# Performance work log

Measured on AMD Instinct MI355X. Metric: run time of the kernel, lower is better.

## Reference

```python
import jax, jax.numpy as jnp
import numpy as np


def setup_inputs() -> dict:
    key = jax.random.key(0)
    ks = jax.random.split(key, 5)
    b, l, ns, ni, d = 128, 64, 32, 16, 256
    scale = 1.0 / np.sqrt(d)
    return {
        "token_features": jax.random.normal(ks[0], (b, l, d), jnp.float32),
        "w_route_ws": jax.random.normal(ks[1], (l, ns, d), jnp.float32) * scale,
        "w_pose_ws": jax.random.normal(ks[2], (l, ns, d, d), jnp.float32) * scale,
        "w_route_si": jax.random.normal(ks[3], (ns, ni, d), jnp.float32) * scale,
        "w_pose_si": jax.random.normal(ks[4], (ns, ni, d, d), jnp.float32) * scale,
    }


def reference(token_features, w_route_ws, w_pose_ws, w_route_si, w_pose_si):
    d_model = token_features.shape[-1]

    # ---- route words -> slots ----
    # token activations ('norm' strategy): mean over d_model -> (b, l)
    a_words = jnp.sum(token_features, axis=-1) / d_model
    # routing logits (b, l, n_slot_caps), softmax over slot caps
    c_ws = jax.nn.softmax(jnp.einsum('lnj,blj->bln', w_route_ws, token_features), axis=-1)
    weighted_c = jnp.einsum('bls,bl->bs', c_ws, a_words)            # (b, ns)
    a_slots = weighted_c / jnp.sum(a_words, axis=-1, keepdims=True)  # (b, ns)
    # pose votes (b, l, ns, d) then weighted aggregation + divisive normalization
    u_hat_slots = jnp.einsum('lnij,blj->blni', w_pose_ws, token_features)
    u_slots = jnp.einsum('bls,bl,blsk->bsk', c_ws, a_words, u_hat_slots) / weighted_c[:, :, None]

    # ---- route slots -> intents ----
    c_si = jax.nn.softmax(jnp.einsum('sij,bsj->bsi', w_route_si, u_slots), axis=-1)
    weighted_c2 = jnp.einsum('bsi,bs->bi', c_si, a_slots)            # (b, ni)
    a_intents = weighted_c2 / jnp.sum(a_slots, axis=-1, keepdims=True)
    u_hat_intents = jnp.einsum('sijk,bsk->bsik', w_pose_si, u_slots)  # (b, ns, ni, d)
    u_intents = jnp.einsum('bsi,bs,bsik->bik', c_si, a_slots, u_hat_intents) / weighted_c2[:, :, None]

    return a_slots, u_slots, a_intents, u_intents
```

## Files before the change

kernel.cpp:

```cpp
#include <hip/hip_runtime.h>
#include <math.h>

#define B  128
#define L  64
#define NS 32
#define NI 16
#define D  256

typedef __attribute__((ext_vector_type(8))) short bf16x8;
typedef __attribute__((ext_vector_type(4))) float f32x4;

__device__ __forceinline__ float wave_reduce_sum(float v) {
#pragma unroll
  for (int off = 32; off; off >>= 1) v += __shfl_xor(v, off, 64);
  return v;
}
__device__ __forceinline__ float wave_reduce_max(float v) {
#pragma unroll
  for (int off = 32; off; off >>= 1) v = fmaxf(v, __shfl_xor(v, off, 64));
  return v;
}

__device__ __forceinline__ uint cvt_pk_bf16(float a, float b) {
  uint r;
  asm("v_cvt_pk_bf16_f32 %0, %1, %2" : "=v"(r) : "v"(a), "v"(b));
  return r;
}
__device__ __forceinline__ void split4(float4 v, uint2& h, uint2& lo) {
  h.x = cvt_pk_bf16(v.x, v.y);
  h.y = cvt_pk_bf16(v.z, v.w);
  float h0 = __uint_as_float(h.x << 16);
  float h1 = __uint_as_float(h.x & 0xFFFF0000u);
  float h2 = __uint_as_float(h.y << 16);
  float h3 = __uint_as_float(h.y & 0xFFFF0000u);
  lo.x = cvt_pk_bf16(v.x - h0, v.y - h1);
  lo.y = cvt_pk_bf16(v.z - h2, v.w - h3);
}

__device__ __forceinline__ void dma16(const void* g, void* l) {
  __builtin_amdgcn_global_load_lds(
      (const __attribute__((address_space(1))) void*)g,
      (__attribute__((address_space(3))) void*)l, 16, 0, 0);
}

__device__ __forceinline__ int swzA(int row, int kcol) {
  int byte = (row << 7) + (kcol << 1);
  byte ^= (row & 7) << 4;
  return byte >> 1;
}

__global__ __launch_bounds__(256) void kx_split(
    const float* __restrict__ tf, ushort* __restrict__ xh,
    ushort* __restrict__ xl) {
  int tile = blockIdx.x;
  int l  = tile >> 2;
  int jc = (tile & 3) * 64;
  int t  = threadIdx.x;
  int row = t >> 1;
  int k0  = (t & 1) * 32;
  const float* src = tf + ((size_t)row * L + l) * D + jc + k0;
  ushort* ht = xh + (size_t)tile * 8192;
  ushort* lt = xl + (size_t)tile * 8192;
#pragma unroll
  for (int c = 0; c < 8; ++c) {
    float4 v = *(const float4*)(src + c * 4);
    uint2 h, lo;
    split4(v, h, lo);
    int ix = swzA(row, k0 + c * 4);
    *(uint2*)&ht[ix] = h;
    *(uint2*)&lt[ix] = lo;
  }
}

__global__ __launch_bounds__(256) void k1_route_words(
    const float* __restrict__ tf, const float* __restrict__ wr,
    float* __restrict__ wlsT, float* __restrict__ a_words) {
  int bl = blockIdx.x;
  int b  = bl >> 6;
  int l  = bl & (L - 1);
  int t  = threadIdx.x;
  int wave = t >> 6, lane = t & 63;
  __shared__ float sx[D];
  __shared__ float slog[NS];
  __shared__ float s_aw;
  sx[t] = tf[bl * D + t];
  __syncthreads();
  const float* wbase = wr + l * NS * D;
#pragma unroll
  for (int r = 0; r < 8; ++r) {
    int n = wave * 8 + r;
    const float* w = wbase + n * D;
    float p = 0.f;
#pragma unroll
    for (int jj = 0; jj < 4; ++jj) {
      int j = lane + jj * 64;
      p = fmaf(w[j], sx[j], p);
    }
    p = wave_reduce_sum(p);
    if (lane == 0) slog[n] = p;
  }
  if (wave == 0) {
    float p = sx[lane] + sx[lane + 64] + sx[lane + 128] + sx[lane + 192];
    p = wave_reduce_sum(p);
    if (lane == 0) s_aw = p * (1.f / D);
  }
  __syncthreads();
  if (wave == 0) {
    float aw = s_aw;
    float v = (lane < NS) ? slog[lane] : -INFINITY;
    float m = wave_reduce_max(v);
    float e = (lane < NS) ? __expf(v - m) : 0.f;
    float s = wave_reduce_sum(e);
    if (lane < NS) wlsT[(l * NS + lane) * B + b] = (e / s) * aw;
    if (lane == 0) a_words[bl] = aw;
  }
}

__global__ __launch_bounds__(64) void k2_slots_agg(
    const float* __restrict__ wlsT, const float* __restrict__ a_words,
    float* __restrict__ weighted_c, float* __restrict__ a_slots) {
  int b = blockIdx.x;
  int lane = threadIdx.x;
  float aw = a_words[b * L + lane];
  float sa = wave_reduce_sum(aw);
  if (lane < NS) {
    float wc = 0.f;
    for (int l = 0; l < L; ++l) wc += wlsT[(l * NS + lane) * B + b];
    weighted_c[b * NS + lane] = wc;
    a_slots[b * NS + lane] = wc / sa;
  }
}

__global__ __launch_bounds__(256) void k3_mfma(
    const ushort* __restrict__ xh, const ushort* __restrict__ xl,
    const float* __restrict__ wp, const float* __restrict__ wlsT,
    float* __restrict__ part, int nsplit) {
  __shared__ ushort Ah[8192], Al[8192];
  __shared__ float sw[128];

  int bx  = blockIdx.x;
  int sp  = bx % nsplit;
  int rem = bx / nsplit;
  int it  = rem & 3;
  int s   = rem >> 2;
  int i0  = it * 64;
  int lchunk = L / nsplit;
  int l0     = sp * lchunk;
  int steps  = lchunk * 4;

  int t = threadIdx.x;
  int lane = t & 63, wv = t >> 6;
  int wm = wv >> 1, wn = wv & 1;
  int fr = lane & 15, q = lane >> 4;

  f32x4 P[4][2], R[4][2];
#pragma unroll
  for (int mi = 0; mi < 4; ++mi)
#pragma unroll
    for (int ni = 0; ni < 2; ++ni) { P[mi][ni] = (f32x4)0.f; R[mi][ni] = (f32x4)0.f; }

  for (int step = 0; step < steps; ++step) {
    int l   = l0 + (step >> 2);
    int jci = step & 3;
    size_t tile = ((size_t)l * 4 + jci) * 8192;
    const ushort* th = xh + tile;
    const ushort* tl = xl + tile;
#pragma unroll
    for (int ii = 0; ii < 4; ++ii) {
      int ofs = (wv * 4 + ii) * 512;
      dma16(th + ofs + lane * 8, &Ah[ofs]);
      dma16(tl + ofs + lane * 8, &Al[ofs]);
    }
    int jc = jci * 64;
    float4 rW[8];
    const float* wb = wp + ((size_t)l * NS + s) * (D * D) + jc + q * 8;
#pragma unroll
    for (int ni = 0; ni < 2; ++ni) {
      const float* wr_ = wb + (size_t)(i0 + wn * 32 + ni * 16 + fr) * D;
#pragma unroll
      for (int k2 = 0; k2 < 2; ++k2) {
        rW[(ni * 2 + k2) * 2 + 0] = *(const float4*)(wr_ + k2 * 32);
        rW[(ni * 2 + k2) * 2 + 1] = *(const float4*)(wr_ + k2 * 32 + 4);
      }
    }
    if (jci == 0 && t < 128) sw[t] = wlsT[((size_t)l * NS + s) * B + t];
    __syncthreads();

    bf16x8 bh[2][2], bl[2][2];
#pragma unroll
    for (int ni = 0; ni < 2; ++ni)
#pragma unroll
      for (int k2 = 0; k2 < 2; ++k2) {
        uint2 h0, e0, h1, e1;
        split4(rW[(ni * 2 + k2) * 2 + 0], h0, e0);
        split4(rW[(ni * 2 + k2) * 2 + 1], h1, e1);
        uint4 hu = {h0.x, h0.y, h1.x, h1.y};
        uint4 lu = {e0.x, e0.y, e1.x, e1.y};
        bh[ni][k2] = __builtin_bit_cast(bf16x8, hu);
        bl[ni][k2] = __builtin_bit_cast(bf16x8, lu);
      }
#pragma unroll
    for (int k2 = 0; k2 < 2; ++k2) {
      int kb = k2 * 32 + q * 8;
#pragma unroll
      for (int mi = 0; mi < 4; ++mi) {
        int ix = swzA(wm * 64 + mi * 16 + fr, kb);
        bf16x8 ah = *(const bf16x8*)&Ah[ix];
        bf16x8 al = *(const bf16x8*)&Al[ix];
#pragma unroll
        for (int ni = 0; ni < 2; ++ni) {
          P[mi][ni] = __builtin_amdgcn_mfma_f32_16x16x32_bf16(ah, bh[ni][k2], P[mi][ni], 0, 0, 0);
          P[mi][ni] = __builtin_amdgcn_mfma_f32_16x16x32_bf16(ah, bl[ni][k2], P[mi][ni], 0, 0, 0);
          P[mi][ni] = __builtin_amdgcn_mfma_f32_16x16x32_bf16(al, bh[ni][k2], P[mi][ni], 0, 0, 0);
        }
      }
    }
    if (jci == 3) {
#pragma unroll
      for (int mi = 0; mi < 4; ++mi) {
        f32x4 s4 = *(const f32x4*)&sw[wm * 64 + mi * 16 + q * 4];
#pragma unroll
        for (int ni = 0; ni < 2; ++ni) {
          R[mi][ni] += s4 * P[mi][ni];
          P[mi][ni] = (f32x4)0.f;
        }
      }
    }
    __syncthreads();
  }

  float* pout = part + ((size_t)sp * NS + s) * (B * D);
#pragma unroll
  for (int mi = 0; mi < 4; ++mi)
#pragma unroll
    for (int ni = 0; ni < 2; ++ni) {
      int col = i0 + wn * 32 + ni * 16 + fr;
#pragma unroll
      for (int r = 0; r < 4; ++r) {
        int bb = wm * 64 + mi * 16 + q * 4 + r;
        pout[(size_t)bb * D + col] = R[mi][ni][r];
      }
    }
}

__global__ __launch_bounds__(256) void k3r_reduce(
    const float* __restrict__ part, const float* __restrict__ wc,
    float* __restrict__ u_slots, int nsplit) {
  int idx = blockIdx.x * 256 + threadIdx.x;
  int i  = idx & (D - 1);
  int sb = idx >> 8;
  int b  = sb & (B - 1);
  int s  = sb >> 7;
  float v = 0.f;
  for (int sp = 0; sp < nsplit; ++sp)
    v += part[(size_t)sp * (NS * B * D) + idx];
  u_slots[((size_t)b * NS + s) * D + i] = v / wc[b * NS + s];
}

__global__ __launch_bounds__(64) void k4_route_si(
    const float* __restrict__ u_slots, const float* __restrict__ wr_si,
    const float* __restrict__ a_slots, float* __restrict__ w2) {
  int bs = blockIdx.x;
  int s  = bs & (NS - 1);
  int lane = threadIdx.x;
  __shared__ float su[D];
  __shared__ float slog[NI];
#pragma unroll
  for (int jj = 0; jj < 4; ++jj) su[lane + jj * 64] = u_slots[bs * D + lane + jj * 64];
  __syncthreads();
  for (int i = 0; i < NI; ++i) {
    const float* w = wr_si + (s * NI + i) * D;
    float p = 0.f;
#pragma unroll
    for (int jj = 0; jj < 4; ++jj) {
      int j = lane + jj * 64;
      p = fmaf(w[j], su[j], p);
    }
    p = wave_reduce_sum(p);
    if (lane == 0) slog[i] = p;
  }
  __syncthreads();
  float v = (lane < NI) ? slog[lane] : -INFINITY;
  float m = wave_reduce_max(v);
  float e = (lane < NI) ? __expf(v - m) : 0.f;
  float ssum = wave_reduce_sum(e);
  if (lane < NI) w2[bs * NI + lane] = (e / ssum) * a_slots[bs];
}

__global__ __launch_bounds__(64) void k5_intents_agg(
    const float* __restrict__ w2, const float* __restrict__ a_slots,
    float* __restrict__ wc2, float* __restrict__ a_intents) {
  int b = blockIdx.x;
  int lane = threadIdx.x;
  float as = (lane < NS) ? a_slots[b * NS + lane] : 0.f;
  float sas = wave_reduce_sum(as);
  if (lane < NI) {
    float wc = 0.f;
    for (int s = 0; s < NS; ++s) wc += w2[(b * NS + s) * NI + lane];
    wc2[b * NI + lane] = wc;
    a_intents[b * NI + lane] = wc / sas;
  }
}

__global__ __launch_bounds__(256) void k6_wsum(
    const float* __restrict__ wps, float* __restrict__ wsum) {
  __shared__ float red[4][D];
  int si = blockIdx.x;
  int t  = threadIdx.x;
  int k4 = (t & 63) * 4;
  int jg = t >> 6;
  const float* base = wps + (size_t)si * D * D;
  float4 acc = {0.f, 0.f, 0.f, 0.f};
  for (int j = jg; j < D; j += 4) {
    float4 v = *(const float4*)(base + (size_t)j * D + k4);
    acc.x += v.x; acc.y += v.y; acc.z += v.z; acc.w += v.w;
  }
  *(float4*)&red[jg][k4] = acc;
  __syncthreads();
  wsum[si * D + t] = (red[0][t] + red[1][t]) + (red[2][t] + red[3][t]);
}

__global__ __launch_bounds__(256) void k7_uintents(
    const float* __restrict__ u_slots, const float* __restrict__ w2,
    const float* __restrict__ wsum, const float* __restrict__ wc2,
    float* __restrict__ u_intents) {
  int bi = blockIdx.x;
  int b = bi >> 4, i = bi & (NI - 1);
  int k = threadIdx.x;
  float acc = 0.f;
  for (int s = 0; s < NS; ++s) {
    float w = w2[(b * NS + s) * NI + i];
    acc = fmaf(w * u_slots[(b * NS + s) * D + k], wsum[(s * NI + i) * D + k], acc);
  }
  u_intents[bi * D + k] = acc / wc2[bi];
}

extern "C" void kernel_launch(void* const* d_in, const int* in_sizes, int n_in,
                              void* d_out, int out_size, void* d_ws, size_t ws_size,
                              hipStream_t stream) {
  const float* tf    = (const float*)d_in[0];
  const float* wr_ws = (const float*)d_in[1];
  const float* wp_ws = (const float*)d_in[2];
  const float* wr_si = (const float*)d_in[3];
  const float* wp_si = (const float*)d_in[4];

  float* out       = (float*)d_out;
  float* a_slots   = out;
  float* u_slots   = a_slots + B * NS;
  float* a_intents = u_slots + B * NS * D;
  float* u_intents = a_intents + B * NI;

  float* ws         = (float*)d_ws;
  float* wlsT       = ws;
  float* a_words    = wlsT + L * NS * B;
  float* weighted_c = a_words + B * L;
  float* w2         = weighted_c + B * NS;
  float* wc2        = w2 + B * NS * NI;
  float* wsum       = wc2 + B * NI;
  ushort* xh        = (ushort*)(wsum + NS * NI * D);
  ushort* xl        = xh + (size_t)L * 4 * 8192;
  float*  part      = (float*)(xl + (size_t)L * 4 * 8192);

  const size_t base_f  = 473088 + 1048576 * 2 / 2 * 2;
  const size_t chunk_f = (size_t)NS * B * D;
  size_t avail_f = ws_size / sizeof(float);
  int nsplit = 1;
  if (avail_f >= base_f + 4 * chunk_f)      nsplit = 4;
  else if (avail_f >= base_f + 2 * chunk_f) nsplit = 2;

  kx_split<<<L * 4, 256, 0, stream>>>(tf, xh, xl);
  k1_route_words<<<B * L, 256, 0, stream>>>(tf, wr_ws, wlsT, a_words);
  k2_slots_agg<<<B, 64, 0, stream>>>(wlsT, a_words, weighted_c, a_slots);
  k3_mfma<<<NS * 4 * nsplit, 256, 0, stream>>>(xh, xl, wp_ws, wlsT, part, nsplit);
  k3r_reduce<<<(NS * B * D) / 256, 256, 0, stream>>>(part, weighted_c, u_slots, nsplit);
  k6_wsum<<<NS * NI, 256, 0, stream>>>(wp_si, wsum);
  k4_route_si<<<B * NS, 64, 0, stream>>>(u_slots, wr_si, a_slots, w2);
  k5_intents_agg<<<B, 64, 0, stream>>>(w2, a_slots, wc2, a_intents);
  k7_uintents<<<B * NI, 256, 0, stream>>>(u_slots, w2, wsum, wc2, u_intents);
}
```

Measured before the change: 297.0 us.

## Double-buffer k3 MFMA tiles with async DMA and split batch across blocks

Rewrites the main pose-vote GEMM kernel to double-buffer both the token tiles and the weight tiles in LDS, loading weights through async DMA with an XOR swizzle instead of through registers. It also splits the batch dimension into two halves per block, doubling the grid, preloads all routing coefficients for the L-chunk up front, and remaps block indices so related blocks land on the same XCD. The aim is to overlap global loads with MFMA work and raise occupancy (launch bounds of 2 blocks per CU). In exchange the weight tiles are now read twice, once per batch-half block, and LDS use per block grows.

```diff
diff --git a/kernel.cpp b/kernel.cpp
--- a/kernel.cpp
+++ b/kernel.cpp
@@ -131,115 +131,124 @@
   }
 }
 
-__global__ __launch_bounds__(256) void k3_mfma(
+__global__ __launch_bounds__(256, 2) void k3_mfma(
     const ushort* __restrict__ xh, const ushort* __restrict__ xl,
     const float* __restrict__ wp, const float* __restrict__ wlsT,
     float* __restrict__ part, int nsplit) {
-  __shared__ ushort Ah[8192], Al[8192];
-  __shared__ float sw[128];
-
-  int bx  = blockIdx.x;
-  int sp  = bx % nsplit;
-  int rem = bx / nsplit;
-  int it  = rem & 3;
-  int s   = rem >> 2;
-  int i0  = it * 64;
-  int lchunk = L / nsplit;
-  int l0     = sp * lchunk;
+  __shared__ ushort Ah[2][4096], Al[2][4096];
+  __shared__ float  Wt[2][4096];
+  __shared__ float  swl[4096];
+
+  int bx    = blockIdx.x;
+  int xcd   = bx & 7;
+  int bh    = (bx >> 3) & 1;
+  int chunk = bx >> 4;
+  int pidx  = chunk * 8 + xcd;
+  int sp = pidx % nsplit;
+  int rr = pidx / nsplit;
+  int it = rr & 3, s = rr >> 2;
+  int i0 = it * 64;
+  int lchunk = L / nsplit, l0 = sp * lchunk;
   int steps  = lchunk * 4;
 
-  int t = threadIdx.x;
-  int lane = t & 63, wv = t >> 6;
-  int wm = wv >> 1, wn = wv & 1;
+  int t = threadIdx.x, lane = t & 63, wv = t >> 6;
   int fr = lane & 15, q = lane >> 4;
 
-  f32x4 P[4][2], R[4][2];
-#pragma unroll
-  for (int mi = 0; mi < 4; ++mi)
-#pragma unroll
-    for (int ni = 0; ni < 2; ++ni) { P[mi][ni] = (f32x4)0.f; R[mi][ni] = (f32x4)0.f; }
-
-  for (int step = 0; step < steps; ++step) {
-    int l   = l0 + (step >> 2);
-    int jci = step & 3;
-    size_t tile = ((size_t)l * 4 + jci) * 8192;
+  int wofs[4];
+#pragma unroll
+  for (int wi = 0; wi < 4; ++wi) {
+    int row  = (wv * 4 + wi) * 4 + (lane >> 4);
+    int soff = ((lane & 15) * 16) ^ ((row & 7) << 4);
+    wofs[wi] = row * 1024 + soff;
+  }
+  int aofs = wv * 1024 + lane * 8;
+
+  for (int of = t; of < lchunk * 64; of += 256) {
+    int li = of >> 6, b = of & 63;
+    swl[of] = wlsT[((size_t)(l0 + li) * NS + s) * B + bh * 64 + b];
+  }
+  asm volatile("s_waitcnt vmcnt(0) lgkmcnt(0)" ::: "memory");
+  __builtin_amdgcn_s_barrier();
+
+  f32x4 P[4], R[4];
+#pragma unroll
+  for (int mi = 0; mi < 4; ++mi) { P[mi] = (f32x4)0.f; R[mi] = (f32x4)0.f; }
+
+  auto issue = [&](int step) {
+    int cs = step < steps ? step : steps - 1;
+    int pb = step & 1;
+    int l = l0 + (cs >> 2), jci = cs & 3;
+    size_t tile = ((size_t)l * 4 + jci) * 8192 + (size_t)bh * 4096;
     const ushort* th = xh + tile;
     const ushort* tl = xl + tile;
-#pragma unroll
-    for (int ii = 0; ii < 4; ++ii) {
-      int ofs = (wv * 4 + ii) * 512;
-      dma16(th + ofs + lane * 8, &Ah[ofs]);
-      dma16(tl + ofs + lane * 8, &Al[ofs]);
-    }
-    int jc = jci * 64;
-    float4 rW[8];
-    const float* wb = wp + ((size_t)l * NS + s) * (D * D) + jc + q * 8;
-#pragma unroll
-    for (int ni = 0; ni < 2; ++ni) {
-      const float* wr_ = wb + (size_t)(i0 + wn * 32 + ni * 16 + fr) * D;
-#pragma unroll
-      for (int k2 = 0; k2 < 2; ++k2) {
-        rW[(ni * 2 + k2) * 2 + 0] = *(const float4*)(wr_ + k2 * 32);
-        rW[(ni * 2 + k2) * 2 + 1] = *(const float4*)(wr_ + k2 * 32 + 4);
+    dma16(th + aofs,       &Ah[pb][wv * 1024]);
+    dma16(th + aofs + 512, &Ah[pb][wv * 1024 + 512]);
+    dma16(tl + aofs,       &Al[pb][wv * 1024]);
+    dma16(tl + aofs + 512, &Al[pb][wv * 1024 + 512]);
+    const char* wbase = (const char*)(wp + ((size_t)l * NS + s) * (D * D) +
+                                      (size_t)i0 * D + jci * 64);
+#pragma unroll
+    for (int wi = 0; wi < 4; ++wi)
+      dma16(wbase + wofs[wi], (char*)&Wt[pb][0] + (wv * 4 + wi) * 1024);
+  };
+
+  issue(0);
+  for (int step = 0; step < steps; ++step) {
+    issue(step + 1);
+    asm volatile("s_waitcnt vmcnt(8)" ::: "memory");
+    __builtin_amdgcn_s_barrier();
+    int pb = step & 1;
+    int wrow = wv * 16 + fr;
+    int wkey = (wrow & 7) << 4;
+    const char* wb = (const char*)&Wt[pb][0];
+    bf16x8 fh[2], fl[2];
+#pragma unroll
+    for (int k2 = 0; k2 < 2; ++k2) {
+      int base = wrow * 256 + k2 * 128 + q * 32;
+      float4 w0 = *(const float4*)(wb + ((base) ^ wkey));
+      float4 w1 = *(const float4*)(wb + ((base + 16) ^ wkey));
+      uint2 h0, e0, h1, e1;
+      split4(w0, h0, e0);
+      split4(w1, h1, e1);
+      uint4 hu = {h0.x, h0.y, h1.x, h1.y};
+      uint4 lu = {e0.x, e0.y, e1.x, e1.y};
+      fh[k2] = __builtin_bit_cast(bf16x8, hu);
+      fl[k2] = __builtin_bit_cast(bf16x8, lu);
+    }
+#pragma unroll
+    for (int k2 = 0; k2 < 2; ++k2) {
+#pragma unroll
+      for (int mi = 0; mi < 4; ++mi) {
+        int arow  = mi * 16 + fr;
+        int abyte = (arow * 128 + (k2 * 32 + q * 8) * 2) ^ ((arow & 7) << 4);
+        bf16x8 ah = *(const bf16x8*)((const char*)&Ah[pb][0] + abyte);
+        bf16x8 al = *(const bf16x8*)((const char*)&Al[pb][0] + abyte);
+        P[mi] = __builtin_amdgcn_mfma_f32_16x16x32_bf16(ah, fh[k2], P[mi], 0, 0, 0);
+        P[mi] = __builtin_amdgcn_mfma_f32_16x16x32_bf16(ah, fl[k2], P[mi], 0, 0, 0);
+        P[mi] = __builtin_amdgcn_mfma_f32_16x16x32_bf16(al, fh[k2], P[mi], 0, 0, 0);
       }
     }
-    if (jci == 0 && t < 128) sw[t] = wlsT[((size_t)l * NS + s) * B + t];
-    __syncthreads();
-
-    bf16x8 bh[2][2], bl[2][2];
-#pragma unroll
-    for (int ni = 0; ni < 2; ++ni)
-#pragma unroll
-      for (int k2 = 0; k2 < 2; ++k2) {
-        uint2 h0, e0, h1, e1;
-        split4(rW[(ni * 2 + k2) * 2 + 0], h0, e0);
-        split4(rW[(ni * 2 + k2) * 2 + 1], h1, e1);
-        uint4 hu = {h0.x, h0.y, h1.x, h1.y};
-        uint4 lu = {e0.x, e0.y, e1.x, e1.y};
-        bh[ni][k2] = __builtin_bit_cast(bf16x8, hu);
-        bl[ni][k2] = __builtin_bit_cast(bf16x8, lu);
+    if ((step & 3) == 3) {
+      int sl = step >> 2;
+#pragma unroll
+      for (int mi = 0; mi < 4; ++mi) {
+        f32x4 s4 = *(const f32x4*)&swl[sl * 64 + mi * 16 + q * 4];
+        R[mi] += s4 * P[mi];
+        P[mi] = (f32x4)0.f;
       }
-#pragma unroll
-    for (int k2 = 0; k2 < 2; ++k2) {
-      int kb = k2 * 32 + q * 8;
-#pragma unroll
-      for (int mi = 0; mi < 4; ++mi) {
-        int ix = swzA(wm * 64 + mi * 16 + fr, kb);
-        bf16x8 ah = *(const bf16x8*)&Ah[ix];
-        bf16x8 al = *(const bf16x8*)&Al[ix];
-#pragma unroll
-        for (int ni = 0; ni < 2; ++ni) {
-          P[mi][ni] = __builtin_amdgcn_mfma_f32_16x16x32_bf16(ah, bh[ni][k2], P[mi][ni], 0, 0, 0);
-          P[mi][ni] = __builtin_amdgcn_mfma_f32_16x16x32_bf16(ah, bl[ni][k2], P[mi][ni], 0, 0, 0);
-          P[mi][ni] = __builtin_amdgcn_mfma_f32_16x16x32_bf16(al, bh[ni][k2], P[mi][ni], 0, 0, 0);
-        }
-      }
-    }
-    if (jci == 3) {
-#pragma unroll
-      for (int mi = 0; mi < 4; ++mi) {
-        f32x4 s4 = *(const f32x4*)&sw[wm * 64 + mi * 16 + q * 4];
-#pragma unroll
-        for (int ni = 0; ni < 2; ++ni) {
-          R[mi][ni] += s4 * P[mi][ni];
-          P[mi][ni] = (f32x4)0.f;
-        }
-      }
-    }
-    __syncthreads();
+    }
+    asm volatile("s_waitcnt lgkmcnt(0)" ::: "memory");
+    __builtin_amdgcn_s_barrier();
   }
 
   float* pout = part + ((size_t)sp * NS + s) * (B * D);
+  int col = i0 + wv * 16 + fr;
 #pragma unroll
   for (int mi = 0; mi < 4; ++mi)
 #pragma unroll
-    for (int ni = 0; ni < 2; ++ni) {
-      int col = i0 + wn * 32 + ni * 16 + fr;
-#pragma unroll
-      for (int r = 0; r < 4; ++r) {
-        int bb = wm * 64 + mi * 16 + q * 4 + r;
-        pout[(size_t)bb * D + col] = R[mi][ni][r];
-      }
+    for (int e = 0; e < 4; ++e) {
+      int bb = bh * 64 + mi * 16 + q * 4 + e;
+      pout[(size_t)bb * D + col] = R[mi][e];
     }
 }
 
@@ -361,7 +370,7 @@
   ushort* xl        = xh + (size_t)L * 4 * 8192;
   float*  part      = (float*)(xl + (size_t)L * 4 * 8192);
 
-  const size_t base_f  = 473088 + 1048576 * 2 / 2 * 2;
+  const size_t base_f  = 473088 + 2097152;
   const size_t chunk_f = (size_t)NS * B * D;
   size_t avail_f = ws_size / sizeof(float);
   int nsplit = 1;
@@ -371,7 +380,7 @@
   kx_split<<<L * 4, 256, 0, stream>>>(tf, xh, xl);
   k1_route_words<<<B * L, 256, 0, stream>>>(tf, wr_ws, wlsT, a_words);
   k2_slots_agg<<<B, 64, 0, stream>>>(wlsT, a_words, weighted_c, a_slots);
-  k3_mfma<<<NS * 4 * nsplit, 256, 0, stream>>>(xh, xl, wp_ws, wlsT, part, nsplit);
+  k3_mfma<<<NS * 4 * 2 * nsplit, 256, 0, stream>>>(xh, xl, wp_ws, wlsT, part, nsplit);
   k3r_reduce<<<(NS * B * D) / 256, 256, 0, stream>>>(part, weighted_c, u_slots, nsplit);
   k6_wsum<<<NS * NI, 256, 0, stream>>>(wp_si, wsum);
   k4_route_si<<<B * NS, 64, 0, stream>>>(u_slots, wr_si, a_slots, w2);
```

Result: no change. 296.9 us (-0.0%).
